# Performance work log

Hardware: AMD Instinct MI355X
Metric: run time of the kernel (lower is better)

Reference implementation:

```python
import jax, jax.numpy as jnp
import numpy as np

D_MODEL = 1024
NUM_HEADS = 16
HEAD_DIM = D_MODEL // NUM_HEADS


def setup_inputs() -> dict:
    key = jax.random.key(0)
    ks = jax.random.split(key, 8)
    B, S = 4, 1024
    scale = 1.0 / np.sqrt(D_MODEL)
    return {
        "x": jax.random.normal(ks[0], (B, S, D_MODEL), jnp.float32),
        "tokens": jax.random.normal(ks[1], (B, 1, D_MODEL), jnp.float32),
        "Wq": jax.random.normal(ks[2], (D_MODEL, D_MODEL), jnp.float32) * scale,
        "bq": jnp.zeros((D_MODEL,), jnp.float32),
        "Wk": jax.random.normal(ks[3], (D_MODEL, D_MODEL), jnp.float32) * scale,
        "bk": jnp.zeros((D_MODEL,), jnp.float32),
        "Wv": jax.random.normal(ks[4], (D_MODEL, D_MODEL), jnp.float32) * scale,
        "bv": jnp.zeros((D_MODEL,), jnp.float32),
    }


def _split_heads(t):
    # [B, S, D] -> [B, H, S, hd]
    B, S, _ = t.shape
    return t.reshape(B, S, NUM_HEADS, HEAD_DIM).transpose(0, 2, 1, 3)


def reference(x, tokens, Wq, bq, Wk, bk, Wv, bv):
    # Projections (torch Linear: y = x @ W.T + b)
    Q = _split_heads(x @ Wq.T + bq)          # [B,H,S,hd]
    K = _split_heads(x @ Wk.T + bk)
    V = _split_heads(x @ Wv.T + bv)
    tQ = _split_heads(tokens @ Wq.T + bq)    # [B,H,1,hd] -> broadcast
    tK = _split_heads(tokens @ Wk.T + bk)
    cQ = Q + tQ
    cK = K + tK
    scores = jnp.einsum("bhqd,bhkd->bhqk", cQ, cK) / jnp.sqrt(jnp.float32(HEAD_DIM))
    attn = jax.nn.softmax(scores, axis=-1)
    out = jnp.einsum("bhqk,bhkd->bhqd", attn, V)  # [B,H,S,hd]
    B, H, S, hd = out.shape
    return out.transpose(0, 2, 1, 3).reshape(B, S, D_MODEL)
```

## Files before the change

### kernel.cpp

```cpp
#include <hip/hip_runtime.h>
#include <hip/hip_bf16.h>


typedef __bf16 bf16;
typedef __bf16 bf16x8 __attribute__((ext_vector_type(8)));
typedef float  f32x4  __attribute__((ext_vector_type(4)));

#define LOG2E 1.4426950408889634f

__device__ __forceinline__ void gll16(const void* g, void* l) {
  __builtin_amdgcn_global_load_lds(
      (const __attribute__((address_space(1))) unsigned int*)g,
      (__attribute__((address_space(3))) unsigned int*)l, 16, 0, 0);
}

__device__ __forceinline__ unsigned cvtpk(float a, float b) {
  unsigned r;
  asm("v_cvt_pk_bf16_f32 %0, %1, %2" : "=v"(r) : "v"(a), "v"(b));
  return r;
}

__global__ void prep_kernel(const float* __restrict__ x, const float* __restrict__ tok,
                            const float* __restrict__ wq, const float* __restrict__ wk,
                            const float* __restrict__ wv,
                            bf16* __restrict__ xb, bf16* __restrict__ xt,
                            bf16* __restrict__ wdst) {
  const int bid = blockIdx.x;
  if (bid < 2048) {
    const size_t e = ((size_t)bid * 256 + threadIdx.x) * 8;
    const int b = (int)(e >> 20);
    const int d = (int)(e & 1023);
    const float4 a0 = *(const float4*)(x + e);
    const float4 a1 = *(const float4*)(x + e + 4);
    const float4 t0 = *(const float4*)(tok + b * 1024 + d);
    const float4 t1 = *(const float4*)(tok + b * 1024 + d + 4);
    bf16x8 vb, vt;
    vb[0]=(bf16)a0.x; vb[1]=(bf16)a0.y; vb[2]=(bf16)a0.z; vb[3]=(bf16)a0.w;
    vb[4]=(bf16)a1.x; vb[5]=(bf16)a1.y; vb[6]=(bf16)a1.z; vb[7]=(bf16)a1.w;
    vt[0]=(bf16)(a0.x+t0.x); vt[1]=(bf16)(a0.y+t0.y); vt[2]=(bf16)(a0.z+t0.z); vt[3]=(bf16)(a0.w+t0.w);
    vt[4]=(bf16)(a1.x+t1.x); vt[5]=(bf16)(a1.y+t1.y); vt[6]=(bf16)(a1.z+t1.z); vt[7]=(bf16)(a1.w+t1.w);
    *(bf16x8*)(xb + e) = vb;
    *(bf16x8*)(xt + e) = vt;
  } else {
    const size_t e = ((size_t)(bid - 2048) * 256 + threadIdx.x) * 8;
    const float* src; size_t off;
    if (e < (size_t)(1u<<20))      { src = wq; off = e; }
    else if (e < (size_t)(2u<<20)) { src = wk; off = e - (1u<<20); }
    else                           { src = wv; off = e - (2u<<20); }
    const float4 a0 = *(const float4*)(src + off);
    const float4 a1 = *(const float4*)(src + off + 4);
    bf16x8 v;
    v[0]=(bf16)a0.x; v[1]=(bf16)a0.y; v[2]=(bf16)a0.z; v[3]=(bf16)a0.w;
    v[4]=(bf16)a1.x; v[5]=(bf16)a1.y; v[6]=(bf16)a1.z; v[7]=(bf16)a1.w;
    *(bf16x8*)(wdst + e) = v;
  }
}

__global__ __launch_bounds__(256, 3) void qkv_gemm_kernel(
    const bf16* __restrict__ xt, const bf16* __restrict__ xb,
    const bf16* __restrict__ wq, const bf16* __restrict__ wk, const bf16* __restrict__ wv,
    const float* __restrict__ bq, const float* __restrict__ bk, const float* __restrict__ bv,
    bf16* __restrict__ cq, bf16* __restrict__ ck, bf16* __restrict__ vt)
{
  __shared__ __align__(16) char LDSG[49152];
  char* As = LDSG;
  char* Bs = LDSG + 24576;
  const int t = threadIdx.x, w = t >> 6, l = t & 63, g = l >> 4, c = l & 15;
  const int wr = w >> 1, wc = w & 1;
  const int wgid = blockIdx.x;
  const int xcd = wgid & 7;
  const int p = wgid >> 3;
  const int z = p >> 5;
  const int q = p & 31;
  const bf16 *A, *B; const float* bias; bf16* outp;
  int tm, tn;
  if (z < 2) { tm = xcd * 4 + (q & 3); tn = q >> 2; }
  else       { tm = q >> 2; tn = xcd * 4 + (q & 3); }
  if (z == 0)      { A = xt; B = wq; bias = bq; outp = cq; }
  else if (z == 1) { A = xt; B = wk; bias = bk; outp = ck; }
  else             { A = wv; B = xb; bias = bv; outp = vt; }
  const int m0 = tm * 128, n0 = tn * 128;

  f32x4 acc[4][4] = {};

  const int u = (t & 7) ^ ((t >> 3) & 7);
  const size_t ssw = (size_t)(2 * (t >> 3) + (u >> 2)) * 2048 + (size_t)(u & 3) * 16;
  const char* aga = (const char*)A + (size_t)m0 * 2048 + ssw;
  const char* bga = (const char*)B + (size_t)n0 * 2048 + ssw;

#define GSTAGE(slot, kt)                                                 \
  {                                                                      \
    const size_t ko = (size_t)(kt) * 64;            \
    char* ad = As + (slot) * 8192 + t * 16;                              \
    char* bd = Bs + (slot) * 8192 + t * 16;                              \
    gll16(aga + ko,          ad);                                        \
    gll16(aga + ko + 131072, ad + 4096);               \
    gll16(bga + ko,          bd);                                        \
    gll16(bga + ko + 131072, bd + 4096);                                 \
  }

  GSTAGE(0, 0);
  GSTAGE(1, 1);
  int st = 2;
  int s  = 0;
  for (int kt = 0; kt < 32; ++kt) {
    if (kt < 31) { asm volatile("s_waitcnt vmcnt(4)" ::: "memory"); }
    else         { asm volatile("s_waitcnt vmcnt(0)" ::: "memory"); }
    __builtin_amdgcn_sched_barrier(0);
    __builtin_amdgcn_s_barrier();
    if (kt < 30) GSTAGE(st, kt + 2);

    const char* Ab = As + s * 8192;
    const char* Bb = Bs + s * 8192;
    bf16x8 af[4], bfr[4];
#pragma unroll
    for (int mf = 0; mf < 4; ++mf) {
      const int mrow = wr * 64 + mf * 16 + c;
      af[mf] = *(const bf16x8*)(Ab + (mrow >> 1) * 128 +
                                (((((mrow & 1) << 2) + g) ^ ((mrow >> 1) & 7)) << 4));
    }
#pragma unroll
    for (int nf = 0; nf < 4; ++nf) {
      const int nrow = wc * 64 + nf * 16 + c;
      bfr[nf] = *(const bf16x8*)(Bb + (nrow >> 1) * 128 +
                                 (((((nrow & 1) << 2) + g) ^ ((nrow >> 1) & 7)) << 4));
    }
    __builtin_amdgcn_s_setprio(1);
#pragma unroll
    for (int mf = 0; mf < 4; ++mf)
#pragma unroll
      for (int nf = 0; nf < 4; ++nf)
        acc[mf][nf] = __builtin_amdgcn_mfma_f32_16x16x32_bf16(af[mf], bfr[nf], acc[mf][nf], 0, 0, 0);
    __builtin_amdgcn_s_setprio(0);
    s  = (s  == 2) ? 0 : s + 1;
    st = (st == 2) ? 0 : st + 1;
  }
#undef GSTAGE

  if (z < 2) {
    const float sc = (z == 0) ? 0.125f * LOG2E : 1.0f;
#pragma unroll
    for (int mf = 0; mf < 4; ++mf)
#pragma unroll
      for (int nf = 0; nf < 4; ++nf) {
        const int n = n0 + wc * 64 + nf * 16 + c;
        const int h = n >> 6, d = n & 63;
        const float bsum = 2.0f * bias[n];
#pragma unroll
        for (int r = 0; r < 4; ++r) {
          const int m = m0 + wr * 64 + mf * 16 + g * 4 + r;
          const int b = m >> 10, s2 = m & 1023;
          outp[(((size_t)(b * 16 + h)) * 1024 + s2) * 64 + d] = (bf16)((acc[mf][nf][r] + bsum) * sc);
        }
      }
  } else {
#pragma unroll
    for (int mf = 0; mf < 4; ++mf)
#pragma unroll
      for (int nf = 0; nf < 4; ++nf) {
        const int n = n0 + wc * 64 + nf * 16 + c;
        const int b = n >> 10, s2 = n & 1023;
#pragma unroll
        for (int r = 0; r < 4; ++r) {
          const int m = m0 + wr * 64 + mf * 16 + g * 4 + r;
          const int h = m >> 6, d = m & 63;
          outp[(((size_t)(b * 16 + h)) * 64 + d) * 1024 + s2] = (bf16)(acc[mf][nf][r] + bias[m]);
        }
      }
  }
}

__global__ __launch_bounds__(512) void attn_kernel(
    const bf16* __restrict__ cq, const bf16* __restrict__ ck, const bf16* __restrict__ vt,
    float* __restrict__ out)
{
  __shared__ __align__(16) char LDS[49152];
  const int t = threadIdx.x, w = t >> 6, l = t & 63, g = l >> 4, c = l & 15;
  const int bh = blockIdx.y, qt = blockIdx.x;
  const int b = bh >> 4, h = bh & 15;
  const bf16* cqb = cq + (size_t)bh * 65536;
  const bf16* ckb = ck + (size_t)bh * 65536;
  const bf16* vtb = vt + (size_t)bh * 65536;
  const int q0 = qt * 128 + w * 16;

  bf16x8 qf[2];
#pragma unroll
  for (int kf = 0; kf < 2; ++kf)
    qf[kf] = *(const bf16x8*)(cqb + (size_t)(q0 + c) * 64 + kf * 32 + g * 8);

  f32x4 o[4] = {};
  float m = -INFINITY, lsum = 0.f;

  const int r_ = t >> 3;
  const int sch = (t & 7) ^ (r_ & 7);
  const int kap = ((r_ >> 4) & 1) * 32 + ((r_ >> 2) & 3) * 8 + ((r_ >> 5) & 1) * 4 + (r_ & 3);
  const size_t ksrc = (size_t)kap * 128 + (size_t)sch * 16;
  const size_t vsrc = (size_t)r_ * 2048 + (size_t)sch * 16;

#define STAGE(slot, idx)                                                 \
  {                                                                      \
    const char* kgb = (const char*)ckb + (size_t)(idx) * 8192;           \
    const char* vgb = (const char*)vtb + (size_t)(idx) * 128;            \
    gll16(kgb + ksrc, LDS + (slot) * 8192 + t * 16);                     \
    gll16(vgb + vsrc, LDS + 24576 + (slot) * 8192 + t * 16);             \
  }

  STAGE(0, 0);
  STAGE(1, 1);
  int st = 2;
  int s  = 0;
  for (int idx = 0; idx < 16; ++idx) {
    if (idx < 15) { asm volatile("s_waitcnt vmcnt(2)" ::: "memory"); }
    else          { asm volatile("s_waitcnt vmcnt(0)" ::: "memory"); }
    __builtin_amdgcn_sched_barrier(0);
    __builtin_amdgcn_s_barrier();
    if (idx < 14) STAGE(st, idx + 2);

    const char* Kb = LDS + s * 8192;
    const char* Vb = LDS + 24576 + s * 8192;

    f32x4 sv[4] = {};
#pragma unroll
    for (int kf = 0; kf < 2; ++kf)
#pragma unroll
      for (int nf = 0; nf < 4; ++nf) {
        const int kr = nf * 16 + c;
        bf16x8 kb = *(const bf16x8*)(Kb + kr * 128 + (((kf * 4 + g) ^ (kr & 7)) << 4));
        sv[nf] = __builtin_amdgcn_mfma_f32_16x16x32_bf16(kb, qf[kf], sv[nf], 0, 0, 0);
      }

    float vmax = sv[0][0];
#pragma unroll
    for (int nf = 0; nf < 4; ++nf)
#pragma unroll
      for (int r = 0; r < 4; ++r) vmax = fmaxf(vmax, sv[nf][r]);
    vmax = fmaxf(vmax, __shfl_xor(vmax, 16, 64));
    vmax = fmaxf(vmax, __shfl_xor(vmax, 32, 64));
    if (!__all(vmax - m <= 8.0f)) {
      const float mnew = fmaxf(m, vmax);
      const float alpha = exp2f(m - mnew);
      m = mnew;
      lsum *= alpha;
#pragma unroll
      for (int nd = 0; nd < 4; ++nd) o[nd] *= alpha;
    }

    float p[4][4];
    float ps = 0.f;
#pragma unroll
    for (int nf = 0; nf < 4; ++nf)
#pragma unroll
      for (int r = 0; r < 4; ++r) {
        p[nf][r] = exp2f(sv[nf][r] - m);
        ps += p[nf][r];
      }
    ps += __shfl_xor(ps, 16, 64);
    ps += __shfl_xor(ps, 32, 64);
    lsum += ps;

    union { unsigned u[4]; bf16x8 v; } pa0, pa1;
    pa0.u[0] = cvtpk(p[0][0], p[0][1]); pa0.u[1] = cvtpk(p[0][2], p[0][3]);
    pa0.u[2] = cvtpk(p[2][0], p[2][1]); pa0.u[3] = cvtpk(p[2][2], p[2][3]);
    pa1.u[0] = cvtpk(p[1][0], p[1][1]); pa1.u[1] = cvtpk(p[1][2], p[1][3]);
    pa1.u[2] = cvtpk(p[3][0], p[3][1]); pa1.u[3] = cvtpk(p[3][2], p[3][3]);

#pragma unroll
    for (int kf = 0; kf < 2; ++kf) {
      const bf16x8 pav = kf ? pa1.v : pa0.v;
#pragma unroll
      for (int nd = 0; nd < 4; ++nd) {
        const int vr = nd * 16 + c;
        bf16x8 vb = *(const bf16x8*)(Vb + vr * 128 + (((kf * 4 + g) ^ (vr & 7)) << 4));
        o[nd] = __builtin_amdgcn_mfma_f32_16x16x32_bf16(vb, pav, o[nd], 0, 0, 0);
      }
    }

    s  = (s  == 2) ? 0 : s + 1;
    st = (st == 2) ? 0 : st + 1;
  }
#undef STAGE

  __syncthreads();

  const float inv = 1.0f / lsum;
  {
    char* Ob = LDS;
    const int row = w * 16 + c;
#pragma unroll
    for (int nd = 0; nd < 4; ++nd) {
      f32x4 vo = o[nd] * inv;
      const int pch = (nd * 4 + g) ^ (row & 7);
      *(f32x4*)(Ob + row * 256 + (pch << 4)) = vo;
    }
  }
  __syncthreads();
  {
    const int rr = t >> 2;
    float* orow = out + ((size_t)(b * 1024 + qt * 128 + rr)) * 1024 + h * 64;
#pragma unroll
    for (int i = 0; i < 4; ++i) {
      const int ch = (t & 3) + i * 4;
      f32x4 v = *(const f32x4*)(LDS + rr * 256 + ((ch ^ (rr & 7)) << 4));
      *(f32x4*)(orow + ch * 4) = v;
    }
  }
}

extern "C" void kernel_launch(void* const* d_in, const int* in_sizes, int n_in,
                              void* d_out, int out_size, void* d_ws, size_t ws_size,
                              hipStream_t stream) {
  const float* x   = (const float*)d_in[0];
  const float* tok = (const float*)d_in[1];
  const float* Wq  = (const float*)d_in[2];
  const float* bq  = (const float*)d_in[3];
  const float* Wk  = (const float*)d_in[4];
  const float* bk  = (const float*)d_in[5];
  const float* Wv  = (const float*)d_in[6];
  const float* bv  = (const float*)d_in[7];
  float* out = (float*)d_out;
  char* ws = (char*)d_ws;
  bf16* xt  = (bf16*)(ws + (size_t)0);
  bf16* xb  = (bf16*)(ws + ((size_t)8  << 20));
  bf16* wqb = (bf16*)(ws + ((size_t)16 << 20));
  bf16* wkb = (bf16*)(ws + ((size_t)18 << 20));
  bf16* wvb = (bf16*)(ws + ((size_t)20 << 20));
  bf16* cqw = (bf16*)(ws + ((size_t)22 << 20));
  bf16* ckw = (bf16*)(ws + ((size_t)30 << 20));
  bf16* vtw = (bf16*)(ws + ((size_t)38 << 20));

  prep_kernel<<<dim3(3584), dim3(256), 0, stream>>>(x, tok, Wq, Wk, Wv, xb, xt, wqb);
  qkv_gemm_kernel<<<dim3(768), dim3(256), 0, stream>>>(
      xt, xb, wqb, wkb, wvb, bq, bk, bv, cqw, ckw, vtw);
  attn_kernel<<<dim3(8, 64), dim3(512), 0, stream>>>(cqw, ckw, vtw, out);
}
```

Measured before the change: 81.91 us.

## Remap attention blocks per XCD, add MFMA priority hints, tree-reduce max/sum

The attention grid becomes 1D, and workgroup IDs are remapped so all 8 query tiles of a given batch-head land on the same XCD. Those tiles then share K/V reads in that XCD's L2. s_setprio raises wave priority around the two MFMA phases so matrix work from different waves interleaves better with softmax VALU work. The row max and row sum reductions become balanced trees, which shortens the dependency chains. The softmax results should be unchanged, apart from float summation order in the row sum.

```diff
diff --git a/kernel.cpp b/kernel.cpp
--- a/kernel.cpp
+++ b/kernel.cpp
@@ -176,7 +176,11 @@
 {
   __shared__ __align__(16) char LDS[49152];
   const int t = threadIdx.x, w = t >> 6, l = t & 63, g = l >> 4, c = l & 15;
-  const int bh = blockIdx.y, qt = blockIdx.x;
+  const int wgid = blockIdx.x;
+  const int xcd = wgid & 7;
+  const int p_ = wgid >> 3;
+  const int bh = xcd * 8 + (p_ >> 3);
+  const int qt = p_ & 7;
   const int b = bh >> 4, h = bh & 15;
   const bf16* cqb = cq + (size_t)bh * 65536;
   const bf16* ckb = ck + (size_t)bh * 65536;
@@ -220,6 +224,7 @@
     const char* Vb = LDS + 24576 + s * 8192;
 
     f32x4 sv[4] = {};
+    __builtin_amdgcn_s_setprio(1);
 #pragma unroll
     for (int kf = 0; kf < 2; ++kf)
 #pragma unroll
@@ -228,12 +233,13 @@
         bf16x8 kb = *(const bf16x8*)(Kb + kr * 128 + (((kf * 4 + g) ^ (kr & 7)) << 4));
         sv[nf] = __builtin_amdgcn_mfma_f32_16x16x32_bf16(kb, qf[kf], sv[nf], 0, 0, 0);
       }
-
-    float vmax = sv[0][0];
-#pragma unroll
-    for (int nf = 0; nf < 4; ++nf)
-#pragma unroll
-      for (int r = 0; r < 4; ++r) vmax = fmaxf(vmax, sv[nf][r]);
+    __builtin_amdgcn_s_setprio(0);
+
+    const float mx0 = fmaxf(fmaxf(sv[0][0], sv[0][1]), fmaxf(sv[0][2], sv[0][3]));
+    const float mx1 = fmaxf(fmaxf(sv[1][0], sv[1][1]), fmaxf(sv[1][2], sv[1][3]));
+    const float mx2 = fmaxf(fmaxf(sv[2][0], sv[2][1]), fmaxf(sv[2][2], sv[2][3]));
+    const float mx3 = fmaxf(fmaxf(sv[3][0], sv[3][1]), fmaxf(sv[3][2], sv[3][3]));
+    float vmax = fmaxf(fmaxf(mx0, mx1), fmaxf(mx2, mx3));
     vmax = fmaxf(vmax, __shfl_xor(vmax, 16, 64));
     vmax = fmaxf(vmax, __shfl_xor(vmax, 32, 64));
     if (!__all(vmax - m <= 8.0f)) {
@@ -246,14 +252,16 @@
     }
 
     float p[4][4];
-    float ps = 0.f;
 #pragma unroll
     for (int nf = 0; nf < 4; ++nf)
 #pragma unroll
-      for (int r = 0; r < 4; ++r) {
+      for (int r = 0; r < 4; ++r)
         p[nf][r] = exp2f(sv[nf][r] - m);
-        ps += p[nf][r];
-      }
+    const float s0_ = (p[0][0] + p[0][1]) + (p[0][2] + p[0][3]);
+    const float s1_ = (p[1][0] + p[1][1]) + (p[1][2] + p[1][3]);
+    const float s2_ = (p[2][0] + p[2][1]) + (p[2][2] + p[2][3]);
+    const float s3_ = (p[3][0] + p[3][1]) + (p[3][2] + p[3][3]);
+    float ps = (s0_ + s1_) + (s2_ + s3_);
     ps += __shfl_xor(ps, 16, 64);
     ps += __shfl_xor(ps, 32, 64);
     lsum += ps;
@@ -264,6 +272,7 @@
     pa1.u[0] = cvtpk(p[1][0], p[1][1]); pa1.u[1] = cvtpk(p[1][2], p[1][3]);
     pa1.u[2] = cvtpk(p[3][0], p[3][1]); pa1.u[3] = cvtpk(p[3][2], p[3][3]);
 
+    __builtin_amdgcn_s_setprio(1);
 #pragma unroll
     for (int kf = 0; kf < 2; ++kf) {
       const bf16x8 pav = kf ? pa1.v : pa0.v;
@@ -274,6 +283,7 @@
         o[nd] = __builtin_amdgcn_mfma_f32_16x16x32_bf16(vb, pav, o[nd], 0, 0, 0);
       }
     }
+    __builtin_amdgcn_s_setprio(0);
 
     s  = (s  == 2) ? 0 : s + 1;
     st = (st == 2) ? 0 : st + 1;
@@ -331,5 +341,5 @@
   prep_kernel<<<dim3(3584), dim3(256), 0, stream>>>(x, tok, Wq, Wk, Wv, xb, xt, wqb);
   qkv_gemm_kernel<<<dim3(768), dim3(256), 0, stream>>>(
       xt, xb, wqb, wkb, wvb, bq, bk, bv, cqw, ckw, vtw);
-  attn_kernel<<<dim3(8, 64), dim3(512), 0, stream>>>(cqw, ckw, vtw, out);
-}
+  attn_kernel<<<dim3(512), dim3(512), 0, stream>>>(cqw, ckw, vtw, out);
+}
```

Result: faster. 79.90 us (-2.5%).
